# Kernel optimization log

Hardware: AMD Instinct MI355X
Metric: run time of the kernel (lower is better)

## Reference

```python
import jax, jax.numpy as jnp
import numpy as np
import math

D_MODEL = 1024
NUM_HEADS = 16
D_K = 64
B, T = 2, 2048


def setup_inputs() -> dict:
    key = jax.random.key(0)
    ks = jax.random.split(key, 12)
    s = 0.02
    return {
        "Q": jax.random.normal(ks[0], (B, T, D_MODEL), jnp.float32),
        "K": jax.random.normal(ks[1], (B, T, D_MODEL), jnp.float32),
        "V": jax.random.normal(ks[2], (B, T, D_MODEL), jnp.float32),
        # stacked per-head projection weights: [H, d_model, d_k]
        "Wq": jax.random.normal(ks[3], (NUM_HEADS, D_MODEL, D_K), jnp.float32) * s,
        "bq": jax.random.normal(ks[4], (NUM_HEADS, D_K), jnp.float32) * s,
        "Wk": jax.random.normal(ks[5], (NUM_HEADS, D_MODEL, D_K), jnp.float32) * s,
        "bk": jax.random.normal(ks[6], (NUM_HEADS, D_K), jnp.float32) * s,
        "Wv": jax.random.normal(ks[7], (NUM_HEADS, D_MODEL, D_K), jnp.float32) * s,
        "bv": jax.random.normal(ks[8], (NUM_HEADS, D_K), jnp.float32) * s,
        "Wo": jax.random.normal(ks[9], (D_MODEL, D_MODEL), jnp.float32) * s,
        "bo": jax.random.normal(ks[10], (D_MODEL,), jnp.float32) * s,
    }


def reference(Q, K, V, Wq, bq, Wk, bk, Wv, bv, Wo, bo):
    scale = 1.0 / math.sqrt(D_K)
    # fused batched per-head projections (replaces the Python per-head loop)
    Qh = jnp.einsum("btd,hdk->bhtk", Q, Wq) + bq[None, :, None, :]
    Kh = jnp.einsum("btd,hdk->bhtk", K, Wk) + bk[None, :, None, :]
    Vh = jnp.einsum("btd,hdk->bhtk", V, Wv) + bv[None, :, None, :]
    scores = jnp.einsum("bhtk,bhsk->bhts", Qh, Kh) * scale  # [B,H,T,T]
    attn = jax.nn.softmax(scores, axis=-1)
    ctx = jnp.einsum("bhts,bhsk->bhtk", attn, Vh)  # [B,H,T,d_k]
    # Faithful to the original: plain view of contiguous [B,H,T,d] into
    # [B,T,H*d] WITHOUT transposing head/time (matches torch .view semantics).
    bsz, nt = Q.shape[0], Q.shape[1]
    x = ctx.reshape(bsz, nt, NUM_HEADS * D_K)
    out = x @ Wo.T + bo
    # dropout with p=0.0 is identity; omitted for determinism
    return out
```

## Files before the change

kernel.cpp:

```cpp
#include <hip/hip_runtime.h>
#include <stdint.h>

typedef __attribute__((ext_vector_type(8))) short short8;
typedef __attribute__((ext_vector_type(4))) short short4v;
typedef __attribute__((ext_vector_type(4))) float float4v;

#define MFMA16(a, b, c) __builtin_amdgcn_mfma_f32_16x16x32_bf16((a), (b), (c), 0, 0, 0)

__device__ __forceinline__ ushort f2bf_rne(float f) {
  union { float f; unsigned u; } x; x.f = f;
  unsigned r = x.u + 0x7FFFu + ((x.u >> 16) & 1u);
  return (ushort)(r >> 16);
}
__device__ __forceinline__ ushort f2bf_trunc(float f) {
  union { float f; unsigned u; } x; x.f = f;
  return (ushort)(x.u >> 16);
}
__device__ __forceinline__ void gload16(const ushort* g, ushort* lds) {
  __builtin_amdgcn_global_load_lds(
      (__attribute__((address_space(1))) unsigned int*)g,
      (__attribute__((address_space(3))) unsigned int*)lds, 16, 0, 0);
}

#define CEXP 0.1803368801111204f

__device__ __forceinline__ void transpose64f(const float* __restrict__ in, int is,
                                             ushort* __restrict__ out, int os,
                                             ushort* lds ) {
  const int t = threadIdx.x;
#pragma unroll
  for (int it = 0; it < 2; ++it) {
    int e = it * 2048 + t * 8;
    int r = e >> 6, c = e & 63;
    const float* p = in + (size_t)r * is + c;
    float4 x0 = *(const float4*)p;
    float4 x1 = *(const float4*)(p + 4);
    ushort tv[8] __attribute__((aligned(16))) = {
        f2bf_rne(x0.x), f2bf_rne(x0.y), f2bf_rne(x0.z), f2bf_rne(x0.w),
        f2bf_rne(x1.x), f2bf_rne(x1.y), f2bf_rne(x1.z), f2bf_rne(x1.w)};
    *(uint4*)&lds[r * 72 + c] = *(const uint4*)tv;
  }
  __syncthreads();
  const int cc = t >> 2;
  const int rg = (t & 3) * 16;
  ushort tmp[16] __attribute__((aligned(16)));
#pragma unroll
  for (int i = 0; i < 16; ++i) tmp[i] = lds[(rg + i) * 72 + cc];
  *(uint4*)&out[(size_t)cc * os + rg] = *(const uint4*)&tmp[0];
  *(uint4*)&out[(size_t)cc * os + rg + 8] = *(const uint4*)&tmp[8];
}

__global__ __launch_bounds__(256) void prep_kernel(
    const float* __restrict__ Q, const float* __restrict__ K,
    const float* __restrict__ V, const float* __restrict__ Wo,
    const float* __restrict__ Wq, const float* __restrict__ Wk,
    const float* __restrict__ Wv, ushort* __restrict__ Qb, ushort* __restrict__ Kb,
    ushort* __restrict__ Vb, ushort* __restrict__ WoB, ushort* __restrict__ BtQ,
    ushort* __restrict__ BtK, ushort* __restrict__ BtV) {
  __shared__ ushort lds[64 * 72];
  const int bx = blockIdx.x;
  if (bx < 6656) {
    const float* s;
    ushort* d;
    int i;
    if (bx < 6144) {
      const int plane = bx >> 11;
      s = plane == 0 ? Q : (plane == 1 ? K : V);
      d = plane == 0 ? Qb : (plane == 1 ? Kb : Vb);
      i = ((bx & 2047) * 256 + threadIdx.x) * 8;
    } else {
      s = Wo;
      d = WoB;
      i = ((bx - 6144) * 256 + threadIdx.x) * 8;
    }
    float4 a = *(const float4*)(s + i);
    float4 b = *(const float4*)(s + i + 4);
    ushort t[8] __attribute__((aligned(16))) = {
        f2bf_rne(a.x), f2bf_rne(a.y), f2bf_rne(a.z), f2bf_rne(a.w),
        f2bf_rne(b.x), f2bf_rne(b.y), f2bf_rne(b.z), f2bf_rne(b.w)};
    *(uint4*)(d + i) = *(const uint4*)t;
  } else {
    const int rb = bx - 6656;
    const int dt = rb & 15, h = (rb >> 4) & 15, z = rb >> 8;
    const float* W = z == 0 ? Wq : (z == 1 ? Wk : Wv);
    ushort* Bt = z == 0 ? BtQ : (z == 1 ? BtK : BtV);
    transpose64f(W + h * 65536 + dt * 4096, 64, Bt + h * 65536 + dt * 64, 1024, lds);
  }
}

__global__ __launch_bounds__(256, 2) void repack_w_kernel(
    const float* __restrict__ Wq, const float* __restrict__ Wk,
    const float* __restrict__ Wv, ushort* __restrict__ BtQ, ushort* __restrict__ BtK,
    ushort* __restrict__ BtV) {
  __shared__ ushort lds[64 * 72];
  const float* W = blockIdx.z == 0 ? Wq : (blockIdx.z == 1 ? Wk : Wv);
  ushort* Bt = blockIdx.z == 0 ? BtQ : (blockIdx.z == 1 ? BtK : BtV);
  const int h = blockIdx.y, dt = blockIdx.x;
  transpose64f(W + h * 65536 + dt * 4096, 64, Bt + h * 65536 + dt * 64, 1024, lds);
}

template <int F32>
__device__ __forceinline__ void stage16(const void* G, size_t eoff, ushort* ldst) {
  if (F32) {
    const float* p = (const float*)G + eoff;
    float4 x0 = *(const float4*)p;
    float4 x1 = *(const float4*)(p + 4);
    ushort t[8] __attribute__((aligned(16))) = {
        f2bf_rne(x0.x), f2bf_rne(x0.y), f2bf_rne(x0.z), f2bf_rne(x0.w),
        f2bf_rne(x1.x), f2bf_rne(x1.y), f2bf_rne(x1.z), f2bf_rne(x1.w)};
    *(uint4*)ldst = *(const uint4*)t;
  } else {
    gload16((const ushort*)G + eoff, ldst);
  }
}

template <int AF32, int BF32>
__device__ __forceinline__ void gemm_body_basic(const void* __restrict__ A,
                                                const void* __restrict__ Bt,
                                                const float* __restrict__ bias,
                                                void* __restrict__ C, int cmode,
                                                float ascale, int N, int K, ushort* lA,
                                                ushort* lB) {
  const int tid = threadIdx.x;
  const int l = tid & 63, lane15 = l & 15, quad = l >> 4;
  const int mbase = blockIdx.y * 128, nbase = blockIdx.x * 128;
  const int w = tid >> 6;
  const int wrow = (w >> 1) * 64, wcol = (w & 1) * 64;
  const int e0 = tid * 8;
  const int e1 = 2048 + tid * 8;
  const int r0 = e0 >> 5, c0 = e0 & 31;
  const int r1 = e1 >> 5, c1 = e1 & 31;

  float4v acc[4][4];
#pragma unroll
  for (int i = 0; i < 4; ++i)
#pragma unroll
    for (int j = 0; j < 4; ++j) acc[i][j] = (float4v){0.f, 0.f, 0.f, 0.f};

  stage16<AF32>(A, (size_t)(mbase + r0) * K + c0, &lA[e0]);
  stage16<AF32>(A, (size_t)(mbase + r1) * K + c1, &lA[e1]);
  stage16<BF32>(Bt, (size_t)(nbase + r0) * K + c0, &lB[e0]);
  stage16<BF32>(Bt, (size_t)(nbase + r1) * K + c1, &lB[e1]);
  asm volatile("s_waitcnt vmcnt(0)" ::: "memory");
  __syncthreads();

  int cur = 0;
  for (int kb = 0; kb < K; kb += 32) {
    const int nxt = cur ^ 1;
    if (kb + 32 < K) {
      stage16<AF32>(A, (size_t)(mbase + r0) * K + c0 + kb + 32, &lA[nxt * 4096 + e0]);
      stage16<AF32>(A, (size_t)(mbase + r1) * K + c1 + kb + 32, &lA[nxt * 4096 + e1]);
      stage16<BF32>(Bt, (size_t)(nbase + r0) * K + c0 + kb + 32, &lB[nxt * 4096 + e0]);
      stage16<BF32>(Bt, (size_t)(nbase + r1) * K + c1 + kb + 32, &lB[nxt * 4096 + e1]);
    }
    const ushort* cA = &lA[cur * 4096];
    const ushort* cB = &lB[cur * 4096];
    short8 a[4], b[4];
#pragma unroll
    for (int i = 0; i < 4; ++i) {
      a[i] = *(const short8*)&cA[(wrow + i * 16 + lane15) * 32 + quad * 8];
      b[i] = *(const short8*)&cB[(wcol + i * 16 + lane15) * 32 + quad * 8];
    }
#pragma unroll
    for (int i = 0; i < 4; ++i)
#pragma unroll
      for (int j = 0; j < 4; ++j) acc[i][j] = MFMA16(a[i], b[j], acc[i][j]);
    asm volatile("s_waitcnt vmcnt(0)" ::: "memory");
    __syncthreads();
    cur = nxt;
  }

  if (cmode == 3) {
    __syncthreads();
    uint* sp = (uint*)lA + w * 576;
    const int bb = mbase >> 11;
    const int tb = (mbase & 2047) + wrow;
#pragma unroll
    for (int j = 0; j < 4; ++j) {
      {
        const int n = nbase + wcol + j * 16 + lane15;
        const float bvs = bias[n];
#pragma unroll
        for (int i = 0; i < 4; ++i)
#pragma unroll
          for (int rp = 0; rp < 2; ++rp) {
            const uint lo = f2bf_rne((acc[i][j][2 * rp] + bvs) * ascale);
            const uint hi = f2bf_rne((acc[i][j][2 * rp + 1] + bvs) * ascale);
            sp[36 * lane15 + i * 8 + quad * 2 + rp] = lo | (hi << 16);
          }
      }
#pragma unroll
      for (int t = 0; t < 2; ++t) {
        const int row = t * 8 + (l >> 3);
        const int c = l & 7;
        uint4 d = *(const uint4*)(sp + 36 * row + 4 * c);
        const int ng = nbase + wcol + j * 16 + row;
        ushort* dst = (ushort*)C + ((size_t)(bb * 1024 + ng)) * 2048 + tb + c * 8;
        *(uint4*)dst = d;
      }
    }
    return;
  }

#pragma unroll
  for (int j = 0; j < 4; ++j) {
    const int n = nbase + wcol + j * 16 + lane15;
    const float bvs = bias[n];
#pragma unroll
    for (int i = 0; i < 4; ++i) {
      const int m0 = mbase + wrow + i * 16 + quad * 4;
#pragma unroll
      for (int r = 0; r < 4; ++r) {
        const float val = (acc[i][j][r] + bvs) * ascale;
        if (cmode == 1) {
          const int m = m0 + r;
          const int bb = m >> 11, t = m & 2047;
          ((ushort*)C)[((size_t)(bb * 1024 + n)) * 2048 + t] = f2bf_rne(val);
        } else if (cmode == 2) {
          ((float*)C)[(size_t)(m0 + r) * N + n] = val;
        } else {
          ((ushort*)C)[(size_t)(m0 + r) * N + n] = f2bf_rne(val);
        }
      }
    }
  }
}

__global__ __launch_bounds__(256, 2) void proj3_kernel(
    const ushort* __restrict__ Qb, const ushort* __restrict__ Kb,
    const ushort* __restrict__ Vb, const ushort* __restrict__ BtQ,
    const ushort* __restrict__ BtK, const ushort* __restrict__ BtV,
    const float* __restrict__ bq, const float* __restrict__ bk,
    const float* __restrict__ bv, ushort* __restrict__ Qh, ushort* __restrict__ Kh,
    ushort* __restrict__ Vt) {
  __shared__ ushort lA[8192], lB[8192];
  if (blockIdx.z == 0)
    gemm_body_basic<0, 0>(Qb, BtQ, bq, Qh, 0, CEXP, 1024, 1024, lA, lB);
  else if (blockIdx.z == 1)
    gemm_body_basic<0, 0>(Kb, BtK, bk, Kh, 0, 1.0f, 1024, 1024, lA, lB);
  else
    gemm_body_basic<0, 0>(Vb, BtV, bv, Vt, 3, 1.0f, 1024, 1024, lA, lB);
}

__global__ __launch_bounds__(256, 2) void gemm_out_kernel(
    const ushort* __restrict__ X, const ushort* __restrict__ WoB,
    const float* __restrict__ bo, float* __restrict__ out) {
  __shared__ ushort lA[8192], lB[4096];
  const int tid = threadIdx.x;
  const int l = tid & 63, lane15 = l & 15, quad = l >> 4;
  const int mbase = blockIdx.y * 128, nbase = blockIdx.x * 64;
  const int wv = tid >> 6;
  const int wrow = wv * 32;
  const int e0 = tid * 8;
  const int e1 = 2048 + tid * 8;
  const int r0 = e0 >> 5, c0 = e0 & 31;
  const int r1 = e1 >> 5, c1 = e1 & 31;
  const ushort* Ag0 = X + (size_t)(mbase + r0) * 1024 + c0;
  const ushort* Ag1 = X + (size_t)(mbase + r1) * 1024 + c1;
  const ushort* Bg0 = WoB + (size_t)(nbase + r0) * 1024 + c0;

  float4v acc[2][4];
#pragma unroll
  for (int i = 0; i < 2; ++i)
#pragma unroll
    for (int j = 0; j < 4; ++j) acc[i][j] = (float4v){0.f, 0.f, 0.f, 0.f};

  gload16(Ag0, &lA[e0]);
  gload16(Ag1, &lA[e1]);
  gload16(Bg0, &lB[e0]);
  asm volatile("s_waitcnt vmcnt(0)" ::: "memory");
  __syncthreads();

  int cur = 0;
  for (int kb = 0; kb < 1024; kb += 32) {
    const int nxt = cur ^ 1;
    if (kb + 32 < 1024) {
      gload16(Ag0 + kb + 32, &lA[nxt * 4096 + e0]);
      gload16(Ag1 + kb + 32, &lA[nxt * 4096 + e1]);
      gload16(Bg0 + kb + 32, &lB[nxt * 2048 + e0]);
    }
    const ushort* cA = &lA[cur * 4096];
    const ushort* cB = &lB[cur * 2048];
    short8 a[2], b[4];
#pragma unroll
    for (int i = 0; i < 2; ++i)
      a[i] = *(const short8*)&cA[(wrow + i * 16 + lane15) * 32 + quad * 8];
#pragma unroll
    for (int j = 0; j < 4; ++j)
      b[j] = *(const short8*)&cB[(j * 16 + lane15) * 32 + quad * 8];
#pragma unroll
    for (int i = 0; i < 2; ++i)
#pragma unroll
      for (int j = 0; j < 4; ++j) acc[i][j] = MFMA16(a[i], b[j], acc[i][j]);
    asm volatile("s_waitcnt vmcnt(0)" ::: "memory");
    __syncthreads();
    cur = nxt;
  }

#pragma unroll
  for (int j = 0; j < 4; ++j) {
    const int n = nbase + j * 16 + lane15;
    const float bvs = bo[n];
#pragma unroll
    for (int i = 0; i < 2; ++i) {
      const int m0 = mbase + wrow + i * 16 + quad * 4;
#pragma unroll
      for (int r = 0; r < 4; ++r) out[(size_t)(m0 + r) * 1024 + n] = acc[i][j][r] + bvs;
    }
  }
}

__global__ __launch_bounds__(256, 2) void proj3f_kernel(
    const float* __restrict__ Q, const float* __restrict__ Kin,
    const float* __restrict__ V, const ushort* __restrict__ BtQ,
    const ushort* __restrict__ BtK, const ushort* __restrict__ BtV,
    const float* __restrict__ bq, const float* __restrict__ bk,
    const float* __restrict__ bv, ushort* __restrict__ Qh, ushort* __restrict__ Kh,
    ushort* __restrict__ Vt) {
  __shared__ ushort lA[8192], lB[8192];
  if (blockIdx.z == 0)
    gemm_body_basic<1, 0>(Q, BtQ, bq, Qh, 0, CEXP, 1024, 1024, lA, lB);
  else if (blockIdx.z == 1)
    gemm_body_basic<1, 0>(Kin, BtK, bk, Kh, 0, 1.0f, 1024, 1024, lA, lB);
  else
    gemm_body_basic<1, 0>(V, BtV, bv, Vt, 3, 1.0f, 1024, 1024, lA, lB);
}

__global__ __launch_bounds__(256, 2) void gemm_btf_kernel(
    const ushort* __restrict__ X, const float* __restrict__ Wo,
    const float* __restrict__ bo, float* __restrict__ out) {
  __shared__ ushort lA[8192], lB[8192];
  gemm_body_basic<0, 1>(X, Wo, bo, out, 2, 1.0f, 1024, 1024, lA, lB);
}

__global__ __launch_bounds__(512, 4) void attn_kernel(const ushort* __restrict__ Qh,
                                                      const ushort* __restrict__ Kh,
                                                      const ushort* __restrict__ Vt,
                                                      ushort* __restrict__ ctxout) {
  __shared__ ushort lK[2][64 * 64];
  __shared__ ushort lV[2][64 * 64];
  const int tid = threadIdx.x, l = tid & 63, wv = tid >> 6;
  const int lane15 = l & 15, quad = l >> 4;
  const int bh = blockIdx.x, b = bh >> 4, h = bh & 15;
  const int q0 = blockIdx.y * 128 + wv * 16;

  const int sr = tid >> 3;
  const int scb = (tid & 7) ^ (sr & 7);
  const ushort* Kp = Kh + (size_t)(b * 2048) * 1024 + h * 64;
  const ushort* Vp = Vt + (size_t)(bh * 64) * 2048;
  const ushort* Kg = Kp + (size_t)sr * 1024 + scb * 8;
  const ushort* Vg = Vp + (size_t)sr * 2048 + scb * 8;

  const ushort* qrow = Qh + (size_t)(b * 2048 + q0 + lane15) * 1024 + h * 64;
  const short8 qa0 = *(const short8*)&qrow[quad * 8];
  const short8 qa1 = *(const short8*)&qrow[32 + quad * 8];

  const int xm = lane15 & 7;
  const int fr0 = lane15 * 64 + ((quad ^ xm) * 8);
  const int fr1 = lane15 * 64 + (((quad + 4) ^ xm) * 8);

  const short8 ones = {0x3F80, 0x3F80, 0x3F80, 0x3F80, 0x3F80, 0x3F80, 0x3F80, 0x3F80};

  float4v o[4];
  float4v lf = (float4v){0.f, 0.f, 0.f, 0.f};
#pragma unroll
  for (int i = 0; i < 4; ++i) o[i] = (float4v){0.f, 0.f, 0.f, 0.f};

  gload16(Kg, &lK[0][tid * 8]);
  gload16(Vg, &lV[0][tid * 8]);
  asm volatile("s_waitcnt vmcnt(0)" ::: "memory");
  __syncthreads();

  int cur = 0;
  for (int s0 = 0; s0 < 2048; s0 += 64) {
    if (s0 + 64 < 2048) {
      gload16(Kg + (size_t)(s0 + 64) * 1024, &lK[cur ^ 1][tid * 8]);
      gload16(Vg + (s0 + 64), &lV[cur ^ 1][tid * 8]);
    }
    const ushort* Kl = &lK[cur][0];
    const ushort* Vl = &lV[cur][0];

    float4v sb[4];
    __builtin_amdgcn_s_setprio(1);
#pragma unroll
    for (int i = 0; i < 4; ++i) {
      short8 k0 = *(const short8*)&Kl[i * 1024 + fr0];
      short8 k1 = *(const short8*)&Kl[i * 1024 + fr1];
      float4v c = (float4v){0.f, 0.f, 0.f, 0.f};
      c = MFMA16(k0, qa0, c);
      c = MFMA16(k1, qa1, c);
      sb[i] = c;
    }
    __builtin_amdgcn_s_setprio(0);

    uint wpk[4][2];
#pragma unroll
    for (int i = 0; i < 4; ++i) {
      const float e0 = __builtin_amdgcn_exp2f(sb[i][0]);
      const float e1 = __builtin_amdgcn_exp2f(sb[i][1]);
      const float e2 = __builtin_amdgcn_exp2f(sb[i][2]);
      const float e3 = __builtin_amdgcn_exp2f(sb[i][3]);
      asm("v_cvt_pk_bf16_f32 %0, %1, %2" : "=v"(wpk[i][0]) : "v"(e0), "v"(e1));
      asm("v_cvt_pk_bf16_f32 %0, %1, %2" : "=v"(wpk[i][1]) : "v"(e2), "v"(e3));
    }

    union PK { uint w[4]; short8 v; };
    PK u0, u1;
    {
      uint a0 = wpk[0][0], b0 = wpk[1][0];
      asm("v_permlane32_swap_b32 %0, %1" : "+v"(a0), "+v"(b0));
      asm("v_permlane16_swap_b32 %0, %1" : "+v"(a0), "+v"(b0));
      uint a1 = wpk[0][1], b1 = wpk[1][1];
      asm("v_permlane32_swap_b32 %0, %1" : "+v"(a1), "+v"(b1));
      asm("v_permlane16_swap_b32 %0, %1" : "+v"(a1), "+v"(b1));
      u0.w[0] = a0; u0.w[1] = a1; u0.w[2] = b0; u0.w[3] = b1;
      uint a2 = wpk[2][0], b2 = wpk[3][0];
      asm("v_permlane32_swap_b32 %0, %1" : "+v"(a2), "+v"(b2));
      asm("v_permlane16_swap_b32 %0, %1" : "+v"(a2), "+v"(b2));
      uint a3 = wpk[2][1], b3 = wpk[3][1];
      asm("v_permlane32_swap_b32 %0, %1" : "+v"(a3), "+v"(b3));
      asm("v_permlane16_swap_b32 %0, %1" : "+v"(a3), "+v"(b3));
      u1.w[0] = a2; u1.w[1] = a3; u1.w[2] = b2; u1.w[3] = b3;
    }
    const short8 pa0 = u0.v;
    const short8 pa1 = u1.v;

    __builtin_amdgcn_s_setprio(1);
    lf = MFMA16(pa0, ones, lf);
    lf = MFMA16(pa1, ones, lf);
#pragma unroll
    for (int nf = 0; nf < 4; ++nf) {
      short8 v0 = *(const short8*)&Vl[nf * 1024 + fr0];
      short8 v1 = *(const short8*)&Vl[nf * 1024 + fr1];
      o[nf] = MFMA16(pa0, v0, o[nf]);
      o[nf] = MFMA16(pa1, v1, o[nf]);
    }
    __builtin_amdgcn_s_setprio(0);

    asm volatile("s_waitcnt vmcnt(0)" ::: "memory");
    __syncthreads();
    cur ^= 1;
  }

  float inv[4];
#pragma unroll
  for (int r = 0; r < 4; ++r) inv[r] = (lf[r] > 0.f) ? 1.0f / lf[r] : 0.0f;
  ushort* crow = ctxout + ((size_t)bh * 2048 + q0) * 64;
#pragma unroll
  for (int nf = 0; nf < 4; ++nf)
#pragma unroll
    for (int r = 0; r < 4; ++r)
      crow[(size_t)(quad * 4 + r) * 64 + nf * 16 + lane15] = f2bf_rne(o[nf][r] * inv[r]);
}

extern "C" void kernel_launch(void* const* d_in, const int* in_sizes, int n_in,
                              void* d_out, int out_size, void* d_ws, size_t ws_size,
                              hipStream_t stream) {
  const float* Q = (const float*)d_in[0];
  const float* K = (const float*)d_in[1];
  const float* V = (const float*)d_in[2];
  const float* Wq = (const float*)d_in[3];
  const float* bq = (const float*)d_in[4];
  const float* Wk = (const float*)d_in[5];
  const float* bk = (const float*)d_in[6];
  const float* Wv = (const float*)d_in[7];
  const float* bv = (const float*)d_in[8];
  const float* Wo = (const float*)d_in[9];
  const float* bo = (const float*)d_in[10];
  float* out = (float*)d_out;
  ushort* ws = (ushort*)d_ws;

  if (ws_size >= (58ull << 20)) {
    ushort* Qh = ws;
    ushort* Kh = Qh + (4 << 20);
    ushort* Vt = Kh + (4 << 20);
    ushort* BtQ = Vt + (4 << 20);
    ushort* BtK = BtQ + (1 << 20);
    ushort* BtV = BtK + (1 << 20);
    ushort* X = BtQ;
    ushort* WoB = ws + (16ull << 20);
    ushort* Qb = WoB + (1 << 20);
    ushort* Kb = Qb + (4 << 20);
    ushort* Vb = Kb + (4 << 20);

    prep_kernel<<<dim3(7424), 256, 0, stream>>>(Q, K, V, Wo, Wq, Wk, Wv, Qb, Kb, Vb,
                                                WoB, BtQ, BtK, BtV);
    proj3_kernel<<<dim3(8, 32, 3), 256, 0, stream>>>(Qb, Kb, Vb, BtQ, BtK, BtV, bq, bk,
                                                     bv, Qh, Kh, Vt);
    attn_kernel<<<dim3(32, 16), 512, 0, stream>>>(Qh, Kh, Vt, X);
    gemm_out_kernel<<<dim3(16, 32), 256, 0, stream>>>(X, WoB, bo, out);
  } else {
    ushort* Qh = ws;
    ushort* Kh = Qh + (4 << 20);
    ushort* Vt = Kh + (4 << 20);
    ushort* R = Vt + (4 << 20);
    ushort* BtQ = R;
    ushort* BtK = R + (1 << 20);
    ushort* BtV = R + (2 << 20);
    ushort* X = R;

    repack_w_kernel<<<dim3(16, 16, 3), 256, 0, stream>>>(Wq, Wk, Wv, BtQ, BtK, BtV);
    proj3f_kernel<<<dim3(8, 32, 3), 256, 0, stream>>>(Q, K, V, BtQ, BtK, BtV, bq, bk, bv,
                                                      Qh, Kh, Vt);
    attn_kernel<<<dim3(32, 16), 512, 0, stream>>>(Qh, Kh, Vt, X);
    gemm_btf_kernel<<<dim3(8, 32), 256, 0, stream>>>(X, Wo, bo, out);
  }
}
```

Measured before the change: 220.9 us.

## Swizzle GEMM LDS tiles and remap blocks per XCD for L2 locality

The GEMM staging layout changes so each thread loads a 16-byte chunk whose column is XOR-swizzled by row, and the MFMA operand reads apply the matching swizzle. This is meant to cut LDS bank conflicts on the fragment reads. The projection and output GEMMs also switch to a 1D grid that is remapped so consecutive blocks landing on the same XCD share the same row panel, aiming for better L2 reuse. The swizzle has to stay consistent between the global_load_lds writes and the fragment reads, and the remap assumes blocks are dealt round-robin across 8 XCDs.

New measurement: 215.1 us. 2.7% less time.

```diff
diff --git a/kernel.cpp b/kernel.cpp
--- a/kernel.cpp
+++ b/kernel.cpp
@@ -119,17 +119,18 @@
                                                 const void* __restrict__ Bt,
                                                 const float* __restrict__ bias,
                                                 void* __restrict__ C, int cmode,
-                                                float ascale, int N, int K, ushort* lA,
-                                                ushort* lB) {
+                                                float ascale, int N, int K, int mbase,
+                                                int nbase, ushort* lA, ushort* lB) {
   const int tid = threadIdx.x;
   const int l = tid & 63, lane15 = l & 15, quad = l >> 4;
-  const int mbase = blockIdx.y * 128, nbase = blockIdx.x * 128;
   const int w = tid >> 6;
   const int wrow = (w >> 1) * 64, wcol = (w & 1) * 64;
   const int e0 = tid * 8;
   const int e1 = 2048 + tid * 8;
-  const int r0 = e0 >> 5, c0 = e0 & 31;
-  const int r1 = e1 >> 5, c1 = e1 & 31;
+  const int r0 = tid >> 2;
+  const int r1 = r0 + 64;
+  const int cs = ((tid & 3) ^ (r0 & 3)) * 8;
+  const int rsw = lane15 & 3;
 
   float4v acc[4][4];
 #pragma unroll
@@ -137,10 +138,10 @@
 #pragma unroll
     for (int j = 0; j < 4; ++j) acc[i][j] = (float4v){0.f, 0.f, 0.f, 0.f};
 
-  stage16<AF32>(A, (size_t)(mbase + r0) * K + c0, &lA[e0]);
-  stage16<AF32>(A, (size_t)(mbase + r1) * K + c1, &lA[e1]);
-  stage16<BF32>(Bt, (size_t)(nbase + r0) * K + c0, &lB[e0]);
-  stage16<BF32>(Bt, (size_t)(nbase + r1) * K + c1, &lB[e1]);
+  stage16<AF32>(A, (size_t)(mbase + r0) * K + cs, &lA[e0]);
+  stage16<AF32>(A, (size_t)(mbase + r1) * K + cs, &lA[e1]);
+  stage16<BF32>(Bt, (size_t)(nbase + r0) * K + cs, &lB[e0]);
+  stage16<BF32>(Bt, (size_t)(nbase + r1) * K + cs, &lB[e1]);
   asm volatile("s_waitcnt vmcnt(0)" ::: "memory");
   __syncthreads();
 
@@ -148,18 +149,18 @@
   for (int kb = 0; kb < K; kb += 32) {
     const int nxt = cur ^ 1;
     if (kb + 32 < K) {
-      stage16<AF32>(A, (size_t)(mbase + r0) * K + c0 + kb + 32, &lA[nxt * 4096 + e0]);
-      stage16<AF32>(A, (size_t)(mbase + r1) * K + c1 + kb + 32, &lA[nxt * 4096 + e1]);
-      stage16<BF32>(Bt, (size_t)(nbase + r0) * K + c0 + kb + 32, &lB[nxt * 4096 + e0]);
-      stage16<BF32>(Bt, (size_t)(nbase + r1) * K + c1 + kb + 32, &lB[nxt * 4096 + e1]);
+      stage16<AF32>(A, (size_t)(mbase + r0) * K + cs + kb + 32, &lA[nxt * 4096 + e0]);
+      stage16<AF32>(A, (size_t)(mbase + r1) * K + cs + kb + 32, &lA[nxt * 4096 + e1]);
+      stage16<BF32>(Bt, (size_t)(nbase + r0) * K + cs + kb + 32, &lB[nxt * 4096 + e0]);
+      stage16<BF32>(Bt, (size_t)(nbase + r1) * K + cs + kb + 32, &lB[nxt * 4096 + e1]);
     }
     const ushort* cA = &lA[cur * 4096];
     const ushort* cB = &lB[cur * 4096];
     short8 a[4], b[4];
 #pragma unroll
     for (int i = 0; i < 4; ++i) {
-      a[i] = *(const short8*)&cA[(wrow + i * 16 + lane15) * 32 + quad * 8];
-      b[i] = *(const short8*)&cB[(wcol + i * 16 + lane15) * 32 + quad * 8];
+      a[i] = *(const short8*)&cA[(wrow + i * 16 + lane15) * 32 + (quad ^ rsw) * 8];
+      b[i] = *(const short8*)&cB[(wcol + i * 16 + lane15) * 32 + (quad ^ rsw) * 8];
     }
 #pragma unroll
     for (int i = 0; i < 4; ++i)
@@ -234,30 +235,45 @@
     const float* __restrict__ bv, ushort* __restrict__ Qh, ushort* __restrict__ Kh,
     ushort* __restrict__ Vt) {
   __shared__ ushort lA[8192], lB[8192];
-  if (blockIdx.z == 0)
-    gemm_body_basic<0, 0>(Qb, BtQ, bq, Qh, 0, CEXP, 1024, 1024, lA, lB);
-  else if (blockIdx.z == 1)
-    gemm_body_basic<0, 0>(Kb, BtK, bk, Kh, 0, 1.0f, 1024, 1024, lA, lB);
+  const int lin = blockIdx.x;
+  const int xcd = lin & 7;
+  const int slot = lin >> 3;
+  const int panel = xcd * 12 + (slot >> 3);
+  const int nb = slot & 7;
+  const int zz = panel >> 5;
+  const int yb = panel & 31;
+  const int mbase = yb * 128, nbase = nb * 128;
+  if (zz == 0)
+    gemm_body_basic<0, 0>(Qb, BtQ, bq, Qh, 0, CEXP, 1024, 1024, mbase, nbase, lA, lB);
+  else if (zz == 1)
+    gemm_body_basic<0, 0>(Kb, BtK, bk, Kh, 0, 1.0f, 1024, 1024, mbase, nbase, lA, lB);
   else
-    gemm_body_basic<0, 0>(Vb, BtV, bv, Vt, 3, 1.0f, 1024, 1024, lA, lB);
+    gemm_body_basic<0, 0>(Vb, BtV, bv, Vt, 3, 1.0f, 1024, 1024, mbase, nbase, lA, lB);
 }
 
 __global__ __launch_bounds__(256, 2) void gemm_out_kernel(
     const ushort* __restrict__ X, const ushort* __restrict__ WoB,
     const float* __restrict__ bo, float* __restrict__ out) {
   __shared__ ushort lA[8192], lB[4096];
+  const int lin = blockIdx.x;
+  const int xcd = lin & 7;
+  const int slot = lin >> 3;
+  const int panel = xcd * 4 + (slot >> 4);
+  const int nb = slot & 15;
+  const int mbase = panel * 128, nbase = nb * 64;
   const int tid = threadIdx.x;
   const int l = tid & 63, lane15 = l & 15, quad = l >> 4;
-  const int mbase = blockIdx.y * 128, nbase = blockIdx.x * 64;
   const int wv = tid >> 6;
   const int wrow = wv * 32;
   const int e0 = tid * 8;
   const int e1 = 2048 + tid * 8;
-  const int r0 = e0 >> 5, c0 = e0 & 31;
-  const int r1 = e1 >> 5, c1 = e1 & 31;
-  const ushort* Ag0 = X + (size_t)(mbase + r0) * 1024 + c0;
-  const ushort* Ag1 = X + (size_t)(mbase + r1) * 1024 + c1;
-  const ushort* Bg0 = WoB + (size_t)(nbase + r0) * 1024 + c0;
+  const int r0 = tid >> 2;
+  const int r1 = r0 + 64;
+  const int cs = ((tid & 3) ^ (r0 & 3)) * 8;
+  const int rsw = lane15 & 3;
+  const ushort* Ag0 = X + (size_t)(mbase + r0) * 1024 + cs;
+  const ushort* Ag1 = X + (size_t)(mbase + r1) * 1024 + cs;
+  const ushort* Bg0 = WoB + (size_t)(nbase + r0) * 1024 + cs;
 
   float4v acc[2][4];
 #pragma unroll
@@ -284,10 +300,10 @@
     short8 a[2], b[4];
 #pragma unroll
     for (int i = 0; i < 2; ++i)
-      a[i] = *(const short8*)&cA[(wrow + i * 16 + lane15) * 32 + quad * 8];
+      a[i] = *(const short8*)&cA[(wrow + i * 16 + lane15) * 32 + (quad ^ rsw) * 8];
 #pragma unroll
     for (int j = 0; j < 4; ++j)
-      b[j] = *(const short8*)&cB[(j * 16 + lane15) * 32 + quad * 8];
+      b[j] = *(const short8*)&cB[(j * 16 + lane15) * 32 + (quad ^ rsw) * 8];
 #pragma unroll
     for (int i = 0; i < 2; ++i)
 #pragma unroll
@@ -318,19 +334,21 @@
     const float* __restrict__ bv, ushort* __restrict__ Qh, ushort* __restrict__ Kh,
     ushort* __restrict__ Vt) {
   __shared__ ushort lA[8192], lB[8192];
+  const int mbase = blockIdx.y * 128, nbase = blockIdx.x * 128;
   if (blockIdx.z == 0)
-    gemm_body_basic<1, 0>(Q, BtQ, bq, Qh, 0, CEXP, 1024, 1024, lA, lB);
+    gemm_body_basic<1, 0>(Q, BtQ, bq, Qh, 0, CEXP, 1024, 1024, mbase, nbase, lA, lB);
   else if (blockIdx.z == 1)
-    gemm_body_basic<1, 0>(Kin, BtK, bk, Kh, 0, 1.0f, 1024, 1024, lA, lB);
+    gemm_body_basic<1, 0>(Kin, BtK, bk, Kh, 0, 1.0f, 1024, 1024, mbase, nbase, lA, lB);
   else
-    gemm_body_basic<1, 0>(V, BtV, bv, Vt, 3, 1.0f, 1024, 1024, lA, lB);
+    gemm_body_basic<1, 0>(V, BtV, bv, Vt, 3, 1.0f, 1024, 1024, mbase, nbase, lA, lB);
 }
 
 __global__ __launch_bounds__(256, 2) void gemm_btf_kernel(
     const ushort* __restrict__ X, const float* __restrict__ Wo,
     const float* __restrict__ bo, float* __restrict__ out) {
   __shared__ ushort lA[8192], lB[8192];
-  gemm_body_basic<0, 1>(X, Wo, bo, out, 2, 1.0f, 1024, 1024, lA, lB);
+  const int mbase = blockIdx.y * 128, nbase = blockIdx.x * 128;
+  gemm_body_basic<0, 1>(X, Wo, bo, out, 2, 1.0f, 1024, 1024, mbase, nbase, lA, lB);
 }
 
 __global__ __launch_bounds__(512, 4) void attn_kernel(const ushort* __restrict__ Qh,
@@ -485,10 +503,10 @@
 
     prep_kernel<<<dim3(7424), 256, 0, stream>>>(Q, K, V, Wo, Wq, Wk, Wv, Qb, Kb, Vb,
                                                 WoB, BtQ, BtK, BtV);
-    proj3_kernel<<<dim3(8, 32, 3), 256, 0, stream>>>(Qb, Kb, Vb, BtQ, BtK, BtV, bq, bk,
-                                                     bv, Qh, Kh, Vt);
+    proj3_kernel<<<dim3(768), 256, 0, stream>>>(Qb, Kb, Vb, BtQ, BtK, BtV, bq, bk, bv,
+                                                Qh, Kh, Vt);
     attn_kernel<<<dim3(32, 16), 512, 0, stream>>>(Qh, Kh, Vt, X);
-    gemm_out_kernel<<<dim3(16, 32), 256, 0, stream>>>(X, WoB, bo, out);
+    gemm_out_kernel<<<dim3(512), 256, 0, stream>>>(X, WoB, bo, out);
   } else {
     ushort* Qh = ws;
     ushort* Kh = Qh + (4 << 20);
```
